# Kernel tuning notes

Measured on AMD Instinct MI355X. Metric: run time of the kernel, lower is better.

## Reference

```python
import jax, jax.numpy as jnp
import numpy as np

NFEAT = 256; NHID = 256; NHEADS = 4; DH = NHID // NHEADS; ALPHA = 0.2
B, T, N = 16, 6, 128
NTOT = B * T * N
DEG = 16
E = NTOT * DEG


def setup_inputs() -> dict:
    key = jax.random.key(0)
    ks = jax.random.split(key, 12)
    s = 0.05
    emb = jax.random.normal(ks[0], (B, T, N, NFEAT), jnp.float32)
    nmask = jnp.ones((B, T, N), jnp.float32)
    nodeidx = jnp.arange(NTOT, dtype=jnp.int32)
    # batched-DGL-style edges: random intra-graph edges, avg in-degree DEG
    rng = np.random.default_rng(0)
    TN = T * N
    goff = (np.arange(E) // (TN * DEG)) * TN  # graph block offset per edge
    edge_src = jnp.asarray(rng.integers(0, TN, E) + goff, jnp.int32)
    edge_dst = jnp.asarray(rng.integers(0, TN, E) + goff, jnp.int32)
    tid = jnp.asarray((np.arange(NTOT) // N) % T, jnp.int32)  # turn id per node
    W = jax.random.normal(ks[1], (NFEAT, NHID), jnp.float32) * s
    a_src = jax.random.normal(ks[2], (NHEADS, DH), jnp.float32) * s
    a_dst = jax.random.normal(ks[3], (NHEADS, DH), jnp.float32) * s
    Wz = jax.random.normal(ks[4], (NHID, NHID), jnp.float32) * s
    Uz = jax.random.normal(ks[5], (NHID, NHID), jnp.float32) * s
    Wr = jax.random.normal(ks[6], (NHID, NHID), jnp.float32) * s
    Ur = jax.random.normal(ks[7], (NHID, NHID), jnp.float32) * s
    Wn = jax.random.normal(ks[8], (NHID, NHID), jnp.float32) * s
    Un = jax.random.normal(ks[9], (NHID, NHID), jnp.float32) * s
    bz = jnp.zeros((NHID,), jnp.float32)
    br = jnp.zeros((NHID,), jnp.float32)
    bn = jnp.zeros((NHID,), jnp.float32)
    return dict(emb=emb, nmask=nmask, W=W, a_src=a_src, a_dst=a_dst,
                Wz=Wz, Uz=Uz, Wr=Wr, Ur=Ur, Wn=Wn, Un=Un, bz=bz, br=br, bn=bn,
                nodeidx=nodeidx, edge_src=edge_src, edge_dst=edge_dst, tid=tid)


def reference(emb, nmask, W, a_src, a_dst, Wz, Uz, Wr, Ur, Wn, Un, bz, br, bn,
              nodeidx, edge_src, edge_dst, tid):
    seg_sum = jax.ops.segment_sum
    # set_node_feature: masked utterance embeddings gathered into node order
    feat = (emb * nmask[..., None]).reshape(NTOT, NFEAT)[nodeidx]
    h = feat
    e_attn = None
    # propagation: 6 turn-wise GATGRU updates
    for t in range(T):
        Wh = (h @ W).reshape(NTOT, NHEADS, DH)            # [Ntot,H,Dh]
        es = jnp.sum(Wh * a_src, axis=-1)                 # [Ntot,H]
        ed = jnp.sum(Wh * a_dst, axis=-1)
        logit = jax.nn.leaky_relu(es[edge_src] + ed[edge_dst], ALPHA)  # [E,H]
        # segment softmax over incoming edges of each dst node
        mx = jax.ops.segment_max(logit, edge_dst, num_segments=NTOT)
        mx = jnp.where(jnp.isfinite(mx), mx, 0.0)
        w = jnp.exp(logit - mx[edge_dst])
        den = seg_sum(w, edge_dst, num_segments=NTOT)
        attn = w / (den[edge_dst] + 1e-9)                 # [E,H]
        msg = seg_sum(attn[..., None] * Wh[edge_src], edge_dst,
                      num_segments=NTOT).reshape(NTOT, NHID)
        # GRU update, applied only to nodes of the current turn
        z = jax.nn.sigmoid(msg @ Wz + h @ Uz + bz)
        r = jax.nn.sigmoid(msg @ Wr + h @ Ur + br)
        n = jnp.tanh(msg @ Wn + (r * h) @ Un + bn)
        hn = (1.0 - z) * h + z * n
        h = jnp.where((tid == t)[:, None], hn, h)
        e_attn = attn
    # pooling: attn_score[v] = sum of edge attention into v (copy_e + sum)
    attn_score = seg_sum(e_attn.mean(axis=-1), edge_dst, num_segments=NTOT)
    # read_out_loud: per-graph per-turn softmax-weighted mean, split even/odd turns
    a = jax.nn.softmax(attn_score.reshape(B, T, N), axis=-1)  # softmax within turn
    pooled = jnp.mean(h.reshape(B, T, N, NHID) * a[..., None], axis=2)  # [B,T,nhid]
    r1 = pooled[:, 0::2].sum(axis=1)[:, None, :]  # speaker 1: even turns, [B,1,nhid]
    r2 = pooled[:, 1::2].sum(axis=1)[:, None, :]  # speaker 2: odd turns
    return r1, r2
```

## Files before the change

### kernel.cpp

```cpp
#include <hip/hip_runtime.h>

#define NTOT 12288
#define MAXDEG 64

typedef __attribute__((ext_vector_type(8))) short bf8_t;
typedef __attribute__((ext_vector_type(4))) float f32x4;

__device__ __forceinline__ int turn_row_map(int r, int t) {
  return (r >> 7) * 768 + t * 128 + (r & 127);
}

__device__ __forceinline__ void splitbf(float x, unsigned short& hi, unsigned short& lo) {
  unsigned u = __float_as_uint(x);
  hi = (unsigned short)(u >> 16);
  float fh = __uint_as_float(u & 0xFFFF0000u);
  lo = (unsigned short)(__float_as_uint(x - fh) >> 16);
}
__device__ __forceinline__ float reconf(unsigned short hi, unsigned short lo) {
  return __uint_as_float((unsigned)hi << 16) + __uint_as_float((unsigned)lo << 16);
}
__device__ __forceinline__ uint2 pack4(unsigned short a, unsigned short b,
                                       unsigned short c, unsigned short d) {
  return make_uint2((unsigned)a | ((unsigned)b << 16), (unsigned)c | ((unsigned)d << 16));
}

__device__ __forceinline__ void gemm32x64_k64(
    const unsigned short* __restrict__ ahp, const unsigned short* __restrict__ alp,
    const unsigned short* __restrict__ bhp, const unsigned short* __restrict__ blp,
    unsigned short (&Ah)[32][72], unsigned short (&Al)[32][72],
    unsigned short (&Bh)[64][72], unsigned short (&Bl)[64][72],
    int ar, int aq, int bn_, int bq, int rh, int ch, int quad, int nl,
    f32x4& acc0, f32x4& acc1) {
  for (int k0 = 0; k0 < 256; k0 += 64) {
    *(uint4*)&Ah[ar][aq * 8] = *(const uint4*)(ahp + k0 + aq * 8);
    *(uint4*)&Al[ar][aq * 8] = *(const uint4*)(alp + k0 + aq * 8);
    *(uint4*)&Bh[bn_][bq * 16]     = *(const uint4*)(bhp + k0 + bq * 16);
    *(uint4*)&Bh[bn_][bq * 16 + 8] = *(const uint4*)(bhp + k0 + bq * 16 + 8);
    *(uint4*)&Bl[bn_][bq * 16]     = *(const uint4*)(blp + k0 + bq * 16);
    *(uint4*)&Bl[bn_][bq * 16 + 8] = *(const uint4*)(blp + k0 + bq * 16 + 8);
    __syncthreads();
#pragma unroll
    for (int kk = 0; kk < 64; kk += 32) {
      bf8_t a_h = *(const bf8_t*)&Ah[rh * 16 + nl][kk + quad * 8];
      bf8_t a_l = *(const bf8_t*)&Al[rh * 16 + nl][kk + quad * 8];
      bf8_t bh0 = *(const bf8_t*)&Bh[ch * 32 + nl][kk + quad * 8];
      bf8_t bl0 = *(const bf8_t*)&Bl[ch * 32 + nl][kk + quad * 8];
      bf8_t bh1 = *(const bf8_t*)&Bh[ch * 32 + 16 + nl][kk + quad * 8];
      bf8_t bl1 = *(const bf8_t*)&Bl[ch * 32 + 16 + nl][kk + quad * 8];
      acc0 = __builtin_amdgcn_mfma_f32_16x16x32_bf16(a_h, bh0, acc0, 0, 0, 0);
      acc1 = __builtin_amdgcn_mfma_f32_16x16x32_bf16(a_h, bh1, acc1, 0, 0, 0);
      acc0 = __builtin_amdgcn_mfma_f32_16x16x32_bf16(a_h, bl0, acc0, 0, 0, 0);
      acc1 = __builtin_amdgcn_mfma_f32_16x16x32_bf16(a_h, bl1, acc1, 0, 0, 0);
      acc0 = __builtin_amdgcn_mfma_f32_16x16x32_bf16(a_l, bh0, acc0, 0, 0, 0);
      acc1 = __builtin_amdgcn_mfma_f32_16x16x32_bf16(a_l, bh1, acc1, 0, 0, 0);
    }
    __syncthreads();
  }
}

__global__ void __launch_bounds__(256)
k_prep(const float* __restrict__ emb, const float* __restrict__ nmask,
       const int* __restrict__ nodeidx,
       const float* __restrict__ W, const float* __restrict__ Wz,
       const float* __restrict__ Wr, const float* __restrict__ Wn,
       const float* __restrict__ Uz, const float* __restrict__ Ur,
       const float* __restrict__ Un,
       const int* __restrict__ esrc, const int* __restrict__ edst, int* __restrict__ cnt,
       unsigned short* __restrict__ hbh, unsigned short* __restrict__ hbl,
       unsigned short* __restrict__ wth, unsigned short* __restrict__ wtl,
       unsigned short* __restrict__ adj) {
  int l = blockIdx.x, tid = threadIdx.x;
  if (l < 3072) {
    int i = l * 256 + tid;
    int row = i >> 6;
    int src = nodeidx[row];
    float m = nmask[src];
    float4 v = ((const float4*)emb)[(size_t)src * 64 + (i & 63)];
    v.x *= m; v.y *= m; v.z *= m; v.w *= m;
    unsigned short h0,l0,h1,l1,h2,l2,h3,l3;
    splitbf(v.x,h0,l0); splitbf(v.y,h1,l1); splitbf(v.z,h2,l2); splitbf(v.w,h3,l3);
    int o = row * 256 + (i & 63) * 4;
    *(uint2*)(hbh + o) = pack4(h0,h1,h2,h3);
    *(uint2*)(hbl + o) = pack4(l0,l1,l2,l3);
  } else if (l < 3184) {
    __shared__ float ldt[64][65];
    int bidx = l - 3072;
    int g = bidx >> 4, ti = bidx & 15;
    int tk = (ti & 3) * 64, tn = (ti >> 2) * 64;
    const float* M = g==0?W : g==1?Wz : g==2?Wr : g==3?Wn : g==4?Uz : g==5?Ur : Un;
#pragma unroll
    for (int p = 0; p < 16; p++) {
      int r = p * 4 + (tid >> 6);
      ldt[r][tid & 63] = M[(size_t)(tk + r) * 256 + tn + (tid & 63)];
    }
    __syncthreads();
#pragma unroll
    for (int p = 0; p < 16; p++) {
      int nl_ = p * 4 + (tid >> 6);
      int kl = tid & 63;
      float v = ldt[kl][nl_];
      unsigned short hh, ll; splitbf(v, hh, ll);
      int idx = (g * 256 + tn + nl_) * 256 + tk + kl;
      wth[idx] = hh; wtl[idx] = ll;
    }
  } else {
    int e = (l - 3184) * 256 + tid;
    int d = edst[e];
    int pos = atomicAdd(&cnt[d], 1);
    if (pos < MAXDEG) adj[(size_t)d * MAXDEG + pos] = (unsigned short)esrc[e];
  }
}

__global__ void __launch_bounds__(256)
k_mf5(const unsigned short* __restrict__ aph, const unsigned short* __restrict__ apl,
      const unsigned short* __restrict__ wth, const unsigned short* __restrict__ wtl,
      float* __restrict__ Wh, float* __restrict__ uacc,
      const float* __restrict__ bz, const float* __restrict__ br,
      const float* __restrict__ asrc, const float* __restrict__ adst,
      float* __restrict__ es, float* __restrict__ ed) {
  __shared__ __align__(16) unsigned short Ah[32][72], Al[32][72];
  __shared__ __align__(16) unsigned short Bh[64][72], Bl[64][72];
  __shared__ float esb[32][2], edb[32][2];
  int l = blockIdx.x, tid = threadIdx.x;
  int q = (l < 1536) ? 0 : (l < 3072 ? 1 : 2);
  int bx, by;
  if (q == 0) { bx = (l & 31) >> 3; by = (l >> 5) * 8 + (l & 7); }
  else { int l2 = l - (q == 1 ? 1536 : 3072); bx = (l2 & 63) >> 3; by = (l2 >> 6) * 8 + (l2 & 7); }

  int ar = tid >> 3, aq = tid & 7;
  int bn_ = tid >> 2, bq = tid & 3;
  int gmA = by * 32 + ar;
  int arow;
  if (q == 0) arow = gmA;
  else arow = (gmA / 384) * 768 + (((q == 2) ? 3 : 0) + ((gmA % 384) >> 7)) * 128 + (gmA & 127);
  const unsigned short* ahp = aph + (size_t)arow * 256;
  const unsigned short* alp = apl + (size_t)arow * 256;
  int nbase = (q == 0) ? bx * 64 : 1024 + bx * 64;
  const unsigned short* bhp = wth + (size_t)(nbase + bn_) * 256;
  const unsigned short* blp = wtl + (size_t)(nbase + bn_) * 256;

  int lane = tid & 63, wv = tid >> 6;
  int rh = wv >> 1, ch = wv & 1;
  int quad = lane >> 4, nl = lane & 15;
  f32x4 acc0 = {0.f, 0.f, 0.f, 0.f}, acc1 = {0.f, 0.f, 0.f, 0.f};
  gemm32x64_k64(ahp, alp, bhp, blp, Ah, Al, Bh, Bl, ar, aq, bn_, bq, rh, ch, quad, nl, acc0, acc1);

  int gr = by * 32 + rh * 16 + quad * 4;
  if (q != 0) {
    int rbase = (q == 2) ? 6144 : 0;
#pragma unroll
    for (int r = 0; r < 4; r++) {
      int grr = gr + r;
#pragma unroll
      for (int ct = 0; ct < 2; ct++) {
        float D = (ct == 0) ? acc0[r] : acc1[r];
        int col = bx * 64 + ch * 32 + ct * 16 + nl;
        float bias = (col < 256) ? bz[col] : br[col - 256];
        uacc[(size_t)(rbase + grr) * 512 + col] = D + bias;
      }
    }
  } else {
    int c0 = bx * 64 + ch * 32 + nl, c1 = c0 + 16;
    float a0 = asrc[c0], a1 = asrc[c1], d0 = adst[c0], d1 = adst[c1];
    float pes[4], ped[4];
#pragma unroll
    for (int r = 0; r < 4; r++) {
      int v = gr + r;
      float x0 = acc0[r], x1 = acc1[r];
      Wh[(size_t)v * 256 + c0] = x0;
      Wh[(size_t)v * 256 + c1] = x1;
      pes[r] = x0 * a0 + x1 * a1;
      ped[r] = x0 * d0 + x1 * d1;
    }
#pragma unroll
    for (int m = 1; m < 16; m <<= 1)
#pragma unroll
      for (int r = 0; r < 4; r++) {
        pes[r] += __shfl_xor(pes[r], m);
        ped[r] += __shfl_xor(ped[r], m);
      }
    if (nl == 0)
#pragma unroll
      for (int r = 0; r < 4; r++) {
        esb[rh * 16 + quad * 4 + r][ch] = pes[r];
        edb[rh * 16 + quad * 4 + r][ch] = ped[r];
      }
    __syncthreads();
    if (tid < 32) {
      int m = tid;
      int v = by * 32 + m;
      es[v * 4 + bx] = esb[m][0] + esb[m][1];
      ed[v * 4 + bx] = edb[m][0] + edb[m][1];
    }
  }
}

__global__ void __launch_bounds__(256)
k_upd(const unsigned short* __restrict__ hbh, const unsigned short* __restrict__ hbl,
      const unsigned short* __restrict__ wth, const unsigned short* __restrict__ wtl,
      float* __restrict__ Wh, const float* __restrict__ asrc, const float* __restrict__ adst,
      float* __restrict__ es, float* __restrict__ ed, int tu) {
  __shared__ __align__(16) unsigned short Ah[32][72], Al[32][72];
  __shared__ __align__(16) unsigned short Bh[64][72], Bl[64][72];
  __shared__ float esb[32][2], edb[32][2];
  int l = blockIdx.x, tid = threadIdx.x;
  int bx = (l & 31) >> 3, by = (l >> 5) * 8 + (l & 7);

  int ar = tid >> 3, aq = tid & 7;
  int bn_ = tid >> 2, bq = tid & 3;
  int arow = turn_row_map(by * 32 + ar, tu);
  const unsigned short* ahp = hbh + (size_t)arow * 256;
  const unsigned short* alp = hbl + (size_t)arow * 256;
  int nbase = bx * 64;
  const unsigned short* bhp = wth + (size_t)(nbase + bn_) * 256;
  const unsigned short* blp = wtl + (size_t)(nbase + bn_) * 256;

  int lane = tid & 63, wv = tid >> 6;
  int rh = wv >> 1, ch = wv & 1;
  int quad = lane >> 4, nl = lane & 15;
  f32x4 acc0 = {0.f, 0.f, 0.f, 0.f}, acc1 = {0.f, 0.f, 0.f, 0.f};
  gemm32x64_k64(ahp, alp, bhp, blp, Ah, Al, Bh, Bl, ar, aq, bn_, bq, rh, ch, quad, nl, acc0, acc1);

  int gr = by * 32 + rh * 16 + quad * 4;
  int c0 = bx * 64 + ch * 32 + nl, c1 = c0 + 16;
  float a0 = asrc[c0], a1 = asrc[c1], d0 = adst[c0], d1 = adst[c1];
  float pes[4], ped[4];
#pragma unroll
  for (int r = 0; r < 4; r++) {
    int v = turn_row_map(gr + r, tu);
    float x0 = acc0[r], x1 = acc1[r];
    Wh[(size_t)v * 256 + c0] = x0;
    Wh[(size_t)v * 256 + c1] = x1;
    pes[r] = x0 * a0 + x1 * a1;
    ped[r] = x0 * d0 + x1 * d1;
  }
#pragma unroll
  for (int m = 1; m < 16; m <<= 1)
#pragma unroll
    for (int r = 0; r < 4; r++) {
      pes[r] += __shfl_xor(pes[r], m);
      ped[r] += __shfl_xor(ped[r], m);
    }
  if (nl == 0)
#pragma unroll
    for (int r = 0; r < 4; r++) {
      esb[rh * 16 + quad * 4 + r][ch] = pes[r];
      edb[rh * 16 + quad * 4 + r][ch] = ped[r];
    }
  __syncthreads();
  if (tid < 32) {
    int m = tid;
    int v = turn_row_map(by * 32 + m, tu);
    es[v * 4 + bx] = esb[m][0] + esb[m][1];
    ed[v * 4 + bx] = edb[m][0] + edb[m][1];
  }
}

__global__ void __launch_bounds__(256)
k_attn(const int* __restrict__ cnt, const unsigned short* __restrict__ adj,
       const float* __restrict__ es, const float* __restrict__ ed,
       const float* __restrict__ Wh,
       unsigned short* __restrict__ mbh, unsigned short* __restrict__ mbl, int t) {
  __shared__ float wgs[4][64][4];
  __shared__ unsigned short ssrc[4][64];
  int wv = threadIdx.x >> 6;
  int w = blockIdx.x * 4 + wv;
  int lane = threadIdx.x & 63;
  int v = turn_row_map(w, t);
  int deg = cnt[v];
  if (deg > MAXDEG) deg = MAXDEG;
  const unsigned short* row = adj + (size_t)v * MAXDEG;
  float edq = ed[v * 4 + (lane & 3)];
  float dsum = 0.f;
  int passes = (deg + 15) >> 4;
  for (int p = 0; p < passes; p++) {
    int jj = p * 16 + (lane >> 2);
    if (jj < deg) {
      int s = row[jj];
      float lg = es[s * 4 + (lane & 3)] + edq;
      lg = lg >= 0.f ? lg : 0.2f * lg;
      float wgv = __expf(lg);
      wgs[wv][jj][lane & 3] = wgv;
      if ((lane & 3) == 0) ssrc[wv][jj] = (unsigned short)s;
      dsum += wgv;
    } else {
      wgs[wv][jj][lane & 3] = 0.f;
      if ((lane & 3) == 0) ssrc[wv][jj] = 0;
    }
  }
  dsum += __shfl_xor(dsum, 4);
  dsum += __shfl_xor(dsum, 8);
  dsum += __shfl_xor(dsum, 16);
  dsum += __shfl_xor(dsum, 32);
  float invq = 1.f / (dsum + 1e-9f);
  float myinv = __shfl(invq, lane >> 4);
  float4 acc = make_float4(0.f, 0.f, 0.f, 0.f);
  int deg4 = (deg + 3) & ~3;
  for (int j0 = 0; j0 < deg4; j0 += 4) {
#pragma unroll
    for (int u = 0; u < 4; u++) {
      int s = ssrc[wv][j0 + u];
      float wgv = wgs[wv][j0 + u][lane >> 4];
      float4 x = ((const float4*)Wh)[(size_t)s * 64 + lane];
      acc.x += wgv * x.x; acc.y += wgv * x.y;
      acc.z += wgv * x.z; acc.w += wgv * x.w;
    }
  }
  unsigned short h0,l0,h1,l1,h2,l2,h3,l3;
  splitbf(acc.x * myinv, h0, l0); splitbf(acc.y * myinv, h1, l1);
  splitbf(acc.z * myinv, h2, l2); splitbf(acc.w * myinv, h3, l3);
  int o = w * 256 + lane * 4;
  *(uint2*)(mbh + o) = pack4(h0, h1, h2, h3);
  *(uint2*)(mbl + o) = pack4(l0, l1, l2, l3);
}

__global__ void __launch_bounds__(256)
k_mf2(const unsigned short* __restrict__ mbh, const unsigned short* __restrict__ mbl,
      const unsigned short* __restrict__ wth, const unsigned short* __restrict__ wtl,
      const float* __restrict__ uacc, const float* __restrict__ bn,
      const unsigned short* __restrict__ hbh, const unsigned short* __restrict__ hbl,
      float* __restrict__ g1, unsigned short* __restrict__ rbh, unsigned short* __restrict__ rbl,
      int t) {
  __shared__ __align__(16) unsigned short Ah[32][72], Al[32][72];
  __shared__ __align__(16) unsigned short Bh[64][72], Bl[64][72];
  int l = blockIdx.x, tid = threadIdx.x;
  int bx = (l % 96) >> 3, by = (l / 96) * 8 + (l & 7);

  int ar = tid >> 3, aq = tid & 7;
  int bn_ = tid >> 2, bq = tid & 3;
  int gmA = by * 32 + ar;
  const unsigned short* ahp = mbh + (size_t)gmA * 256;
  const unsigned short* alp = mbl + (size_t)gmA * 256;
  int nbase = 256 + bx * 64;
  const unsigned short* bhp = wth + (size_t)(nbase + bn_) * 256;
  const unsigned short* blp = wtl + (size_t)(nbase + bn_) * 256;

  int lane = tid & 63, wv = tid >> 6;
  int rh = wv >> 1, ch = wv & 1;
  int quad = lane >> 4, nl = lane & 15;
  f32x4 acc0 = {0.f, 0.f, 0.f, 0.f}, acc1 = {0.f, 0.f, 0.f, 0.f};
  gemm32x64_k64(ahp, alp, bhp, blp, Ah, Al, Bh, Bl, ar, aq, bn_, bq, rh, ch, quad, nl, acc0, acc1);

  int gr = by * 32 + rh * 16 + quad * 4;
  int g = bx >> 2;
  int tm3 = t % 3;
  const float* up = uacc + (size_t)(t >= 3 ? 6144 : 0) * 512;
#pragma unroll
  for (int r = 0; r < 4; r++) {
    int grr = gr + r;
    int v = turn_row_map(grr, t);
    int urow = (grr >> 7) * 384 + tm3 * 128 + (grr & 127);
#pragma unroll
    for (int ct = 0; ct < 2; ct++) {
      float D = (ct == 0) ? acc0[r] : acc1[r];
      int c = (bx & 3) * 64 + ch * 32 + ct * 16 + nl;
      if (g == 0) {
        g1[(size_t)grr * 512 + c] = D + up[(size_t)urow * 512 + c];
      } else if (g == 1) {
        float rpre = D + up[(size_t)urow * 512 + 256 + c];
        float rv = 1.f / (1.f + __expf(-rpre));
        int hidx = v * 256 + c;
        float hv = reconf(hbh[hidx], hbl[hidx]);
        float rhv = rv * hv;
        unsigned short hh, ll; splitbf(rhv, hh, ll);
        rbh[grr * 256 + c] = hh; rbl[grr * 256 + c] = ll;
      } else {
        g1[(size_t)grr * 512 + 256 + c] = D + bn[c];
      }
    }
  }
}

__global__ void __launch_bounds__(256)
k_mf3(const unsigned short* __restrict__ rbh, const unsigned short* __restrict__ rbl,
      const unsigned short* __restrict__ wth, const unsigned short* __restrict__ wtl,
      const float* __restrict__ g1,
      unsigned short* __restrict__ hbh, unsigned short* __restrict__ hbl,
      float* __restrict__ outp, int t) {
  __shared__ __align__(16) unsigned short Ah[32][72], Al[32][72];
  __shared__ __align__(16) unsigned short Bh[64][72], Bl[64][72];
  int l = blockIdx.x, tid = threadIdx.x;
  if (l >= 256) {
    ((float4*)outp)[(l - 256) * 256 + tid] = make_float4(0.f, 0.f, 0.f, 0.f);
    return;
  }
  int bx = (l & 31) >> 3, by = (l >> 5) * 8 + (l & 7);

  int ar = tid >> 3, aq = tid & 7;
  int bn_ = tid >> 2, bq = tid & 3;
  int gmA = by * 32 + ar;
  const unsigned short* ahp = rbh + (size_t)gmA * 256;
  const unsigned short* alp = rbl + (size_t)gmA * 256;
  int nbase = 1536 + bx * 64;
  const unsigned short* bhp = wth + (size_t)(nbase + bn_) * 256;
  const unsigned short* blp = wtl + (size_t)(nbase + bn_) * 256;

  int lane = tid & 63, wv = tid >> 6;
  int rh = wv >> 1, ch = wv & 1;
  int quad = lane >> 4, nl = lane & 15;
  f32x4 acc0 = {0.f, 0.f, 0.f, 0.f}, acc1 = {0.f, 0.f, 0.f, 0.f};
  gemm32x64_k64(ahp, alp, bhp, blp, Ah, Al, Bh, Bl, ar, aq, bn_, bq, rh, ch, quad, nl, acc0, acc1);

  int gr = by * 32 + rh * 16 + quad * 4;
#pragma unroll
  for (int r = 0; r < 4; r++) {
    int grr = gr + r;
    int v = turn_row_map(grr, t);
#pragma unroll
    for (int ct = 0; ct < 2; ct++) {
      float D = (ct == 0) ? acc0[r] : acc1[r];
      int c = bx * 64 + ch * 32 + ct * 16 + nl;
      float zpre = g1[(size_t)grr * 512 + c];
      float npre = g1[(size_t)grr * 512 + 256 + c] + D;
      float z = 1.f / (1.f + __expf(-zpre));
      float n = tanhf(npre);
      int hidx = v * 256 + c;
      float hv = reconf(hbh[hidx], hbl[hidx]);
      float hn = (1.f - z) * hv + z * n;
      unsigned short hh, ll; splitbf(hn, hh, ll);
      hbh[hidx] = hh;
      hbl[hidx] = ll;
    }
  }
}

__global__ void __launch_bounds__(256)
k_pool(const int* __restrict__ cnt, const unsigned short* __restrict__ adj,
       const float* __restrict__ es, const float* __restrict__ ed,
       const unsigned short* __restrict__ hbh, const unsigned short* __restrict__ hbl,
       float* __restrict__ out) {
  __shared__ float a[128];
  __shared__ float red[8];
  int bt = blockIdx.x, base = bt * 128, tid = threadIdx.x;
  {
    int n = tid >> 1, v = base + n;
    int deg = cnt[v]; if (deg > MAXDEG) deg = MAXDEG;
    const unsigned short* row = adj + (size_t)v * MAXDEG;
    float part = 0.f;
#pragma unroll
    for (int hh = 0; hh < 2; hh++) {
      int h = (tid & 1) * 2 + hh;
      float edv = ed[v * 4 + h];
      float den = 0.f;
      for (int j0 = 0; j0 < deg; j0 += 4) {
#pragma unroll
        for (int u = 0; u < 4; u++) {
          if (j0 + u < deg) {
            int s = row[j0 + u];
            float lg = es[s * 4 + h] + edv;
            lg = lg >= 0.f ? lg : 0.2f * lg;
            den += __expf(lg);
          }
        }
      }
      part += den / (den + 1e-9f);
    }
    part += __shfl_xor(part, 1);
    if ((tid & 1) == 0) a[n] = 0.25f * part;
  }
  __syncthreads();
  float sv = (tid < 128) ? a[tid] : -1e30f;
  float m = sv;
#pragma unroll
  for (int s = 1; s < 64; s <<= 1) m = fmaxf(m, __shfl_xor(m, s));
  if ((tid & 63) == 0) red[tid >> 6] = m;
  __syncthreads();
  float mx = fmaxf(red[0], red[1]);
  float e = (tid < 128) ? __expf(sv - mx) : 0.f;
  if (tid < 128) a[tid] = e;
  float s_ = e;
#pragma unroll
  for (int s = 1; s < 64; s <<= 1) s_ += __shfl_xor(s_, s);
  if ((tid & 63) == 0) red[4 + (tid >> 6)] = s_;
  __syncthreads();
  float sinv = 1.f / ((red[4] + red[5]) * 128.f);
  float acc = 0.f;
  for (int n = 0; n < 128; n++) {
    int idx = (base + n) * 256 + tid;
    acc += a[n] * reconf(hbh[idx], hbl[idx]);
  }
  int b = bt / 6, tt = bt % 6, spk = tt & 1;
  atomicAdd(&out[spk * 4096 + b * 256 + tid], acc * sinv);
}

extern "C" void kernel_launch(void* const* d_in, const int* in_sizes, int n_in,
                              void* d_out, int out_size, void* d_ws, size_t ws_size,
                              hipStream_t stream) {
  const float* emb    = (const float*)d_in[0];
  const float* nmask  = (const float*)d_in[1];
  const float* W      = (const float*)d_in[2];
  const float* a_src  = (const float*)d_in[3];
  const float* a_dst  = (const float*)d_in[4];
  const float* Wz     = (const float*)d_in[5];
  const float* Uz     = (const float*)d_in[6];
  const float* Wr     = (const float*)d_in[7];
  const float* Ur     = (const float*)d_in[8];
  const float* Wn     = (const float*)d_in[9];
  const float* Un     = (const float*)d_in[10];
  const float* bz     = (const float*)d_in[11];
  const float* br     = (const float*)d_in[12];
  const float* bn     = (const float*)d_in[13];
  const int* nodeidx  = (const int*)d_in[14];
  const int* esrc     = (const int*)d_in[15];
  const int* edst     = (const int*)d_in[16];
  float* out = (float*)d_out;

  char* ws = (char*)d_ws;
  size_t off = 0;
  auto carve = [&](size_t bytes) { char* p = ws + off; off += (bytes + 255) & ~(size_t)255; return p; };
  float* Wh     = (float*)carve((size_t)NTOT * 256 * 4);
  unsigned short* hbh = (unsigned short*)carve((size_t)NTOT * 256 * 2);
  unsigned short* hbl = (unsigned short*)carve((size_t)NTOT * 256 * 2);
  unsigned short* mbh = (unsigned short*)carve(2048 * 256 * 2);
  unsigned short* mbl = (unsigned short*)carve(2048 * 256 * 2);
  unsigned short* rbh = (unsigned short*)carve(2048 * 256 * 2);
  unsigned short* rbl = (unsigned short*)carve(2048 * 256 * 2);
  float* es     = (float*)carve(NTOT * 4 * 4);
  float* ed     = (float*)carve(NTOT * 4 * 4);
  float* g1     = (float*)carve(2048 * 512 * 4);
  float* uacc   = (float*)carve((size_t)12288 * 512 * 4);
  int*   cnt    = (int*)carve(NTOT * 4);
  unsigned short* adj = (unsigned short*)carve((size_t)NTOT * MAXDEG * 2);
  unsigned short* wth = (unsigned short*)carve(1792 * 256 * 2);
  unsigned short* wtl = (unsigned short*)carve(1792 * 256 * 2);
  if (off > ws_size) return;

  hipMemsetAsync(cnt, 0, NTOT * 4, stream);
  k_prep<<<3952, 256, 0, stream>>>(emb, nmask, nodeidx, W, Wz, Wr, Wn, Uz, Ur, Un,
                                   esrc, edst, cnt, hbh, hbl, wth, wtl, adj);
  k_mf5<<<4608, 256, 0, stream>>>(hbh, hbl, wth, wtl, Wh, uacc, bz, br,
                                  a_src, a_dst, es, ed);

  for (int t = 0; t < 6; t++) {
    if (t > 0)
      k_upd<<<256, 256, 0, stream>>>(hbh, hbl, wth, wtl, Wh, a_src, a_dst, es, ed, t - 1);
    k_attn<<<512, 256, 0, stream>>>(cnt, adj, es, ed, Wh, mbh, mbl, t);
    k_mf2<<<768, 256, 0, stream>>>(mbh, mbl, wth, wtl, uacc, bn, hbh, hbl,
                                   g1, rbh, rbl, t);
    k_mf3<<<(t == 5 ? 264 : 256), 256, 0, stream>>>(rbh, rbl, wth, wtl, g1,
                                                    hbh, hbl, out, t);
  }

  k_pool<<<96, 256, 0, stream>>>(cnt, adj, es, ed, hbh, hbl, out);
}
```

Baseline: 337.1 us.

## Widen initial GEMM tiles to 128 columns and fuse pooling scores into final attention

The initial projection GEMM now uses 32x128 output tiles with four MFMA accumulators per wave, halving the block count and reusing each A tile across twice as many columns. The last turn's attention kernel runs over all nodes and writes per-node attention scores, while message aggregation stays limited to nodes of the current turn. The pooling kernel then reads these scores instead of recomputing edge softmax denominators. In exchange, the final attention launch grows sixfold and the widened GEMM uses more registers and shared memory.

```diff
diff --git a/kernel.cpp b/kernel.cpp
--- a/kernel.cpp
+++ b/kernel.cpp
@@ -119,31 +119,57 @@
       const float* __restrict__ asrc, const float* __restrict__ adst,
       float* __restrict__ es, float* __restrict__ ed) {
   __shared__ __align__(16) unsigned short Ah[32][72], Al[32][72];
-  __shared__ __align__(16) unsigned short Bh[64][72], Bl[64][72];
+  __shared__ __align__(16) unsigned short Bh[128][72], Bl[128][72];
   __shared__ float esb[32][2], edb[32][2];
   int l = blockIdx.x, tid = threadIdx.x;
-  int q = (l < 1536) ? 0 : (l < 3072 ? 1 : 2);
+  int q = (l < 768) ? 0 : (l < 1536 ? 1 : 2);
   int bx, by;
-  if (q == 0) { bx = (l & 31) >> 3; by = (l >> 5) * 8 + (l & 7); }
-  else { int l2 = l - (q == 1 ? 1536 : 3072); bx = (l2 & 63) >> 3; by = (l2 >> 6) * 8 + (l2 & 7); }
+  if (q == 0) { bx = (l & 15) >> 3; by = (l >> 4) * 8 + (l & 7); }
+  else { int l2 = l - (q == 1 ? 768 : 1536); bx = (l2 & 31) >> 3; by = (l2 >> 5) * 8 + (l2 & 7); }
 
   int ar = tid >> 3, aq = tid & 7;
-  int bn_ = tid >> 2, bq = tid & 3;
+  int bn_ = tid >> 1, bq = tid & 1;
   int gmA = by * 32 + ar;
   int arow;
   if (q == 0) arow = gmA;
   else arow = (gmA / 384) * 768 + (((q == 2) ? 3 : 0) + ((gmA % 384) >> 7)) * 128 + (gmA & 127);
   const unsigned short* ahp = aph + (size_t)arow * 256;
   const unsigned short* alp = apl + (size_t)arow * 256;
-  int nbase = (q == 0) ? bx * 64 : 1024 + bx * 64;
+  int nbase = (q == 0) ? bx * 128 : 1024 + bx * 128;
   const unsigned short* bhp = wth + (size_t)(nbase + bn_) * 256;
   const unsigned short* blp = wtl + (size_t)(nbase + bn_) * 256;
 
   int lane = tid & 63, wv = tid >> 6;
   int rh = wv >> 1, ch = wv & 1;
   int quad = lane >> 4, nl = lane & 15;
-  f32x4 acc0 = {0.f, 0.f, 0.f, 0.f}, acc1 = {0.f, 0.f, 0.f, 0.f};
-  gemm32x64_k64(ahp, alp, bhp, blp, Ah, Al, Bh, Bl, ar, aq, bn_, bq, rh, ch, quad, nl, acc0, acc1);
+  f32x4 acc[4];
+#pragma unroll
+  for (int ct = 0; ct < 4; ct++) acc[ct] = (f32x4){0.f, 0.f, 0.f, 0.f};
+
+  for (int k0 = 0; k0 < 256; k0 += 64) {
+    *(uint4*)&Ah[ar][aq * 8] = *(const uint4*)(ahp + k0 + aq * 8);
+    *(uint4*)&Al[ar][aq * 8] = *(const uint4*)(alp + k0 + aq * 8);
+#pragma unroll
+    for (int u = 0; u < 4; u++) {
+      *(uint4*)&Bh[bn_][bq * 32 + u * 8] = *(const uint4*)(bhp + k0 + bq * 32 + u * 8);
+      *(uint4*)&Bl[bn_][bq * 32 + u * 8] = *(const uint4*)(blp + k0 + bq * 32 + u * 8);
+    }
+    __syncthreads();
+#pragma unroll
+    for (int kk = 0; kk < 64; kk += 32) {
+      bf8_t a_h = *(const bf8_t*)&Ah[rh * 16 + nl][kk + quad * 8];
+      bf8_t a_l = *(const bf8_t*)&Al[rh * 16 + nl][kk + quad * 8];
+#pragma unroll
+      for (int ct = 0; ct < 4; ct++) {
+        bf8_t bh = *(const bf8_t*)&Bh[ch * 64 + ct * 16 + nl][kk + quad * 8];
+        bf8_t bl = *(const bf8_t*)&Bl[ch * 64 + ct * 16 + nl][kk + quad * 8];
+        acc[ct] = __builtin_amdgcn_mfma_f32_16x16x32_bf16(a_h, bh, acc[ct], 0, 0, 0);
+        acc[ct] = __builtin_amdgcn_mfma_f32_16x16x32_bf16(a_h, bl, acc[ct], 0, 0, 0);
+        acc[ct] = __builtin_amdgcn_mfma_f32_16x16x32_bf16(a_l, bh, acc[ct], 0, 0, 0);
+      }
+    }
+    __syncthreads();
+  }
 
   int gr = by * 32 + rh * 16 + quad * 4;
   if (q != 0) {
@@ -152,25 +178,26 @@
     for (int r = 0; r < 4; r++) {
       int grr = gr + r;
 #pragma unroll
-      for (int ct = 0; ct < 2; ct++) {
-        float D = (ct == 0) ? acc0[r] : acc1[r];
-        int col = bx * 64 + ch * 32 + ct * 16 + nl;
+      for (int ct = 0; ct < 4; ct++) {
+        float D = acc[ct][r];
+        int col = bx * 128 + ch * 64 + ct * 16 + nl;
         float bias = (col < 256) ? bz[col] : br[col - 256];
         uacc[(size_t)(rbase + grr) * 512 + col] = D + bias;
       }
     }
   } else {
-    int c0 = bx * 64 + ch * 32 + nl, c1 = c0 + 16;
-    float a0 = asrc[c0], a1 = asrc[c1], d0 = adst[c0], d1 = adst[c1];
-    float pes[4], ped[4];
-#pragma unroll
-    for (int r = 0; r < 4; r++) {
-      int v = gr + r;
-      float x0 = acc0[r], x1 = acc1[r];
-      Wh[(size_t)v * 256 + c0] = x0;
-      Wh[(size_t)v * 256 + c1] = x1;
-      pes[r] = x0 * a0 + x1 * a1;
-      ped[r] = x0 * d0 + x1 * d1;
+    float pes[4] = {0.f, 0.f, 0.f, 0.f}, ped[4] = {0.f, 0.f, 0.f, 0.f};
+#pragma unroll
+    for (int ct = 0; ct < 4; ct++) {
+      int c = bx * 128 + ch * 64 + ct * 16 + nl;
+      float ac = asrc[c], dc = adst[c];
+#pragma unroll
+      for (int r = 0; r < 4; r++) {
+        float D = acc[ct][r];
+        Wh[(size_t)(gr + r) * 256 + c] = D;
+        pes[r] += D * ac;
+        ped[r] += D * dc;
+      }
     }
 #pragma unroll
     for (int m = 1; m < 16; m <<= 1)
@@ -186,11 +213,11 @@
         edb[rh * 16 + quad * 4 + r][ch] = ped[r];
       }
     __syncthreads();
-    if (tid < 32) {
-      int m = tid;
+    if (tid < 64) {
+      int m = tid & 31, hh = tid >> 5;
       int v = by * 32 + m;
-      es[v * 4 + bx] = esb[m][0] + esb[m][1];
-      ed[v * 4 + bx] = edb[m][0] + edb[m][1];
+      es[v * 4 + bx * 2 + hh] = esb[m][hh];
+      ed[v * 4 + bx * 2 + hh] = edb[m][hh];
     }
   }
 }
@@ -260,13 +287,26 @@
 k_attn(const int* __restrict__ cnt, const unsigned short* __restrict__ adj,
        const float* __restrict__ es, const float* __restrict__ ed,
        const float* __restrict__ Wh,
-       unsigned short* __restrict__ mbh, unsigned short* __restrict__ mbl, int t) {
+       unsigned short* __restrict__ mbh, unsigned short* __restrict__ mbl,
+       float* __restrict__ score, int t, int allnodes) {
   __shared__ float wgs[4][64][4];
   __shared__ unsigned short ssrc[4][64];
+  int gph = blockIdx.x & 15, j = blockIdx.x >> 4;
   int wv = threadIdx.x >> 6;
-  int w = blockIdx.x * 4 + wv;
+  int w = (allnodes ? gph * 768 : gph * 128) + j * 4 + wv;
   int lane = threadIdx.x & 63;
-  int v = turn_row_map(w, t);
+  int v, mrow, storemsg;
+  if (allnodes) {
+    v = w;
+    int bt = v >> 7;
+    int tt = bt % 6;
+    storemsg = (tt == t);
+    mrow = (bt / 6) * 128 + (v & 127);
+  } else {
+    v = turn_row_map(w, t);
+    mrow = w;
+    storemsg = 1;
+  }
   int deg = cnt[v];
   if (deg > MAXDEG) deg = MAXDEG;
   const unsigned short* row = adj + (size_t)v * MAXDEG;
@@ -293,25 +333,33 @@
   dsum += __shfl_xor(dsum, 16);
   dsum += __shfl_xor(dsum, 32);
   float invq = 1.f / (dsum + 1e-9f);
-  float myinv = __shfl(invq, lane >> 4);
-  float4 acc = make_float4(0.f, 0.f, 0.f, 0.f);
-  int deg4 = (deg + 3) & ~3;
-  for (int j0 = 0; j0 < deg4; j0 += 4) {
-#pragma unroll
-    for (int u = 0; u < 4; u++) {
-      int s = ssrc[wv][j0 + u];
-      float wgv = wgs[wv][j0 + u][lane >> 4];
-      float4 x = ((const float4*)Wh)[(size_t)s * 64 + lane];
-      acc.x += wgv * x.x; acc.y += wgv * x.y;
-      acc.z += wgv * x.z; acc.w += wgv * x.w;
-    }
-  }
-  unsigned short h0,l0,h1,l1,h2,l2,h3,l3;
-  splitbf(acc.x * myinv, h0, l0); splitbf(acc.y * myinv, h1, l1);
-  splitbf(acc.z * myinv, h2, l2); splitbf(acc.w * myinv, h3, l3);
-  int o = w * 256 + lane * 4;
-  *(uint2*)(mbh + o) = pack4(h0, h1, h2, h3);
-  *(uint2*)(mbl + o) = pack4(l0, l1, l2, l3);
+  if (allnodes) {
+    float val = dsum * invq;
+    val += __shfl_xor(val, 1);
+    val += __shfl_xor(val, 2);
+    if (lane == 0) score[v] = 0.25f * val;
+  }
+  if (storemsg) {
+    float myinv = __shfl(invq, lane >> 4);
+    float4 acc = make_float4(0.f, 0.f, 0.f, 0.f);
+    int deg4 = (deg + 3) & ~3;
+    for (int j0 = 0; j0 < deg4; j0 += 4) {
+#pragma unroll
+      for (int u = 0; u < 4; u++) {
+        int s = ssrc[wv][j0 + u];
+        float wgv = wgs[wv][j0 + u][lane >> 4];
+        float4 x = ((const float4*)Wh)[(size_t)s * 64 + lane];
+        acc.x += wgv * x.x; acc.y += wgv * x.y;
+        acc.z += wgv * x.z; acc.w += wgv * x.w;
+      }
+    }
+    unsigned short h0,l0,h1,l1,h2,l2,h3,l3;
+    splitbf(acc.x * myinv, h0, l0); splitbf(acc.y * myinv, h1, l1);
+    splitbf(acc.z * myinv, h2, l2); splitbf(acc.w * myinv, h3, l3);
+    int o = mrow * 256 + lane * 4;
+    *(uint2*)(mbh + o) = pack4(h0, h1, h2, h3);
+    *(uint2*)(mbl + o) = pack4(l0, l1, l2, l3);
+  }
 }
 
 __global__ void __launch_bounds__(256)
@@ -425,48 +473,23 @@
 }
 
 __global__ void __launch_bounds__(256)
-k_pool(const int* __restrict__ cnt, const unsigned short* __restrict__ adj,
-       const float* __restrict__ es, const float* __restrict__ ed,
-       const unsigned short* __restrict__ hbh, const unsigned short* __restrict__ hbl,
+k_pool(const float* __restrict__ score,
+       const unsigned short* __restrict__ hbh,
+       const unsigned short* __restrict__ hbl,
        float* __restrict__ out) {
   __shared__ float a[128];
   __shared__ float red[8];
-  int bt = blockIdx.x, base = bt * 128, tid = threadIdx.x;
-  {
-    int n = tid >> 1, v = base + n;
-    int deg = cnt[v]; if (deg > MAXDEG) deg = MAXDEG;
-    const unsigned short* row = adj + (size_t)v * MAXDEG;
-    float part = 0.f;
-#pragma unroll
-    for (int hh = 0; hh < 2; hh++) {
-      int h = (tid & 1) * 2 + hh;
-      float edv = ed[v * 4 + h];
-      float den = 0.f;
-      for (int j0 = 0; j0 < deg; j0 += 4) {
-#pragma unroll
-        for (int u = 0; u < 4; u++) {
-          if (j0 + u < deg) {
-            int s = row[j0 + u];
-            float lg = es[s * 4 + h] + edv;
-            lg = lg >= 0.f ? lg : 0.2f * lg;
-            den += __expf(lg);
-          }
-        }
-      }
-      part += den / (den + 1e-9f);
-    }
-    part += __shfl_xor(part, 1);
-    if ((tid & 1) == 0) a[n] = 0.25f * part;
-  }
-  __syncthreads();
-  float sv = (tid < 128) ? a[tid] : -1e30f;
-  float m = sv;
+  int bt = blockIdx.x;
+  int base = bt * 128;
+  int tid = threadIdx.x;
+  float v = (tid < 128) ? score[base + tid] : -1e30f;
+  float m = v;
 #pragma unroll
   for (int s = 1; s < 64; s <<= 1) m = fmaxf(m, __shfl_xor(m, s));
   if ((tid & 63) == 0) red[tid >> 6] = m;
   __syncthreads();
   float mx = fmaxf(red[0], red[1]);
-  float e = (tid < 128) ? __expf(sv - mx) : 0.f;
+  float e = (tid < 128) ? __expf(v - mx) : 0.f;
   if (tid < 128) a[tid] = e;
   float s_ = e;
 #pragma unroll
@@ -519,6 +542,7 @@
   float* ed     = (float*)carve(NTOT * 4 * 4);
   float* g1     = (float*)carve(2048 * 512 * 4);
   float* uacc   = (float*)carve((size_t)12288 * 512 * 4);
+  float* score  = (float*)carve(NTOT * 4);
   int*   cnt    = (int*)carve(NTOT * 4);
   unsigned short* adj = (unsigned short*)carve((size_t)NTOT * MAXDEG * 2);
   unsigned short* wth = (unsigned short*)carve(1792 * 256 * 2);
@@ -528,18 +552,21 @@
   hipMemsetAsync(cnt, 0, NTOT * 4, stream);
   k_prep<<<3952, 256, 0, stream>>>(emb, nmask, nodeidx, W, Wz, Wr, Wn, Uz, Ur, Un,
                                    esrc, edst, cnt, hbh, hbl, wth, wtl, adj);
-  k_mf5<<<4608, 256, 0, stream>>>(hbh, hbl, wth, wtl, Wh, uacc, bz, br,
+  k_mf5<<<2304, 256, 0, stream>>>(hbh, hbl, wth, wtl, Wh, uacc, bz, br,
                                   a_src, a_dst, es, ed);
 
   for (int t = 0; t < 6; t++) {
     if (t > 0)
       k_upd<<<256, 256, 0, stream>>>(hbh, hbl, wth, wtl, Wh, a_src, a_dst, es, ed, t - 1);
-    k_attn<<<512, 256, 0, stream>>>(cnt, adj, es, ed, Wh, mbh, mbl, t);
+    if (t < 5)
+      k_attn<<<512, 256, 0, stream>>>(cnt, adj, es, ed, Wh, mbh, mbl, score, t, 0);
+    else
+      k_attn<<<3072, 256, 0, stream>>>(cnt, adj, es, ed, Wh, mbh, mbl, score, t, 1);
     k_mf2<<<768, 256, 0, stream>>>(mbh, mbl, wth, wtl, uacc, bn, hbh, hbl,
                                    g1, rbh, rbl, t);
     k_mf3<<<(t == 5 ? 264 : 256), 256, 0, stream>>>(rbh, rbl, wth, wtl, g1,
                                                     hbh, hbl, out, t);
   }
 
-  k_pool<<<96, 256, 0, stream>>>(cnt, adj, es, ed, hbh, hbl, out);
-}
+  k_pool<<<96, 256, 0, stream>>>(score, hbh, hbl, out);
+}
```

Measured after the change: 313.4 us. 1.08x faster.
